# Kernel tuning notes

Hardware: AMD Instinct MI355X
Metric: run time of the kernel (lower is better)

## Reference

```python
import jax, jax.numpy as jnp
import numpy as np

TYPE_PANEL, TYPE_DIALOG, TYPE_CHAR = 1, 2, 3
NUM_ELEMS = 64  # max element index per type (panel count cap per page)
B, S, D = 8, 4096, 768
NPC, NDS = 4, 4  # num_panel_classes, num_dialog_shapes


def setup_inputs() -> dict:
    key = jax.random.key(0)
    ks = jax.random.split(key, 16)
    w = lambda k, shp: jax.random.normal(k, shp, dtype=jnp.float32) * 0.02
    return {
        "element_types": jax.random.randint(ks[0], (B, S), 0, 4, dtype=jnp.int32),
        "element_indices": jax.random.randint(ks[1], (B, S), 0, NUM_ELEMS, dtype=jnp.int32),
        "parent_panel_indices": jax.random.randint(ks[2], (B, S), 0, NUM_ELEMS, dtype=jnp.int32),
        "style_vector": jax.random.normal(ks[3], (B, 4), dtype=jnp.float32),
        "type_emb": w(ks[4], (4, D)),
        "index_emb": w(ks[5], (NUM_ELEMS, D)),
        "parent_emb": w(ks[6], (NUM_ELEMS, D)),
        "style_w": w(ks[7], (4, D)),
        "style_b": jnp.zeros((D,), jnp.float32),
        "ln_g": jnp.ones((D,), jnp.float32),
        "ln_b": jnp.zeros((D,), jnp.float32),
        "panel_w": w(ks[8], (D, NPC + 4)),
        "panel_b": jnp.zeros((NPC + 4,), jnp.float32),
        "dialog_w": w(ks[9], (2 * D, NDS + 4)),
        "dialog_b": jnp.zeros((NDS + 4,), jnp.float32),
        "char_w": w(ks[10], (2 * D, 4)),
        "char_b": jnp.zeros((4,), jnp.float32),
    }


def reference(element_types, element_indices, parent_panel_indices, style_vector,
              type_emb, index_emb, parent_emb, style_w, style_b, ln_g, ln_b,
              panel_w, panel_b, dialog_w, dialog_b, char_w, char_b):
    Bv, Sv = element_types.shape
    # --- TokenLayoutEncoder: embedding sum + style projection + LayerNorm ---
    x = type_emb[element_types] + index_emb[element_indices] + parent_emb[parent_panel_indices]
    x = x + (style_vector @ style_w + style_b)[:, None, :]
    mu = x.mean(-1, keepdims=True)
    var = ((x - mu) ** 2).mean(-1, keepdims=True)
    feats = (x - mu) * jax.lax.rsqrt(var + 1e-5) * ln_g + ln_b  # (B,S,D)

    # --- vectorized _build_parent_remap: orig panel idx -> kept panel order pos ---
    panel_mask = element_types == TYPE_PANEL                      # (B,S)
    kept = (jnp.cumsum(panel_mask, axis=1) - 1).astype(jnp.int32) # order pos of each panel token
    brow = jnp.arange(Bv, dtype=jnp.int32)[:, None]
    col = jnp.where(panel_mask, element_indices, NUM_ELEMS)       # dummy slot for non-panels
    remap = (jnp.full((Bv, NUM_ELEMS + 1), -1, jnp.int32)
             .at[brow, col].max(kept))[:, :NUM_ELEMS]             # (B, NUM_ELEMS)
    # kept panel order pos -> sequence position (for parent feature gather)
    slot = jnp.where(panel_mask, kept, Sv)
    seq_ids = jnp.broadcast_to(jnp.arange(Sv, dtype=jnp.int32), (Bv, Sv))
    pos_table = (jnp.zeros((Bv, Sv + 1), jnp.int32)
                 .at[brow, slot].set(seq_ids))[:, :Sv]            # (B,S)

    # --- parent_pos per token (DIALOG/CHAR only), -1 otherwise ---
    child_mask = (element_types == TYPE_DIALOG) | (element_types == TYPE_CHAR)
    ppos = jnp.where(child_mask,
                     jnp.take_along_axis(remap, parent_panel_indices, axis=1), -1)
    valid = ppos >= 0
    pseq = jnp.take_along_axis(pos_table, jnp.clip(ppos, 0, Sv - 1), axis=1)
    parent_feats = jnp.take_along_axis(feats, pseq[..., None], axis=1)
    parent_feats = parent_feats * valid[..., None].astype(feats.dtype)
    cat = jnp.concatenate([feats, parent_feats], axis=-1)         # (B,S,2D)

    # --- ParallelPredictionHeads, masked per token type ---
    panel_out = (feats @ panel_w + panel_b) * panel_mask[..., None].astype(feats.dtype)
    dmask = ((element_types == TYPE_DIALOG) & valid)[..., None].astype(feats.dtype)
    cmask = ((element_types == TYPE_CHAR) & valid)[..., None].astype(feats.dtype)
    dialog_out = (cat @ dialog_w + dialog_b) * dmask
    char_out = (cat @ char_w + char_b) * cmask
    return panel_out, dialog_out, char_out
```

## Files before the change

### kernel.cpp

```cpp
#include <hip/hip_runtime.h>

#define NB 8
#define NS 4096
#define ND 768

typedef float4 f4;

static __device__ __forceinline__ float wred(float v) {
    v += __shfl_xor(v, 32, 64);
    v += __shfl_xor(v, 16, 64);
    v += __shfl_xor(v, 8, 64);
    v += __shfl_xor(v, 4, 64);
    v += __shfl_xor(v, 2, 64);
    v += __shfl_xor(v, 1, 64);
    return v;
}

static __device__ __forceinline__ f4 ld4(const float* __restrict__ p, int i) {
    return ((const f4*)p)[i];
}

__global__ __launch_bounds__(256) void lp_pre(
    const int* __restrict__ et, const int* __restrict__ ei,
    const float* __restrict__ sv, const float* __restrict__ sw,
    const float* __restrict__ sb,
    int* __restrict__ table, float* __restrict__ sprj)
{
    if (blockIdx.x < 128) {
        int t = blockIdx.x * 256 + threadIdx.x;
        if (et[t] == 1) {
            int b = t >> 12;
            atomicMax(&table[b * 64 + ei[t]], t & (NS - 1));
        }
    } else {
        const int lane = threadIdx.x & 63;
        const int b = (blockIdx.x - 128) * 4 + (threadIdx.x >> 6);
        const float sv0 = sv[b*4+0], sv1 = sv[b*4+1], sv2 = sv[b*4+2], sv3 = sv[b*4+3];
        #pragma unroll
        for (int g = 0; g < 3; ++g) {
            int i = g*64 + lane;
            f4 w0 = ld4(sw, i), w1 = ld4(sw, 192+i), w2 = ld4(sw, 384+i), w3 = ld4(sw, 576+i);
            f4 bb = ld4(sb, i);
            f4 r;
            r.x = bb.x + sv0*w0.x + sv1*w1.x + sv2*w2.x + sv3*w3.x;
            r.y = bb.y + sv0*w0.y + sv1*w1.y + sv2*w2.y + sv3*w3.y;
            r.z = bb.z + sv0*w0.z + sv1*w1.z + sv2*w2.z + sv3*w3.z;
            r.w = bb.w + sv0*w0.w + sv1*w1.w + sv2*w2.w + sv3*w3.w;
            ((f4*)(sprj + b*ND))[i] = r;
        }
    }
}

__global__ __launch_bounds__(256) void lp_parent(
    const int* __restrict__ ei, const int* __restrict__ ppi,
    const float* __restrict__ temb, const float* __restrict__ iemb,
    const float* __restrict__ pemb, const float* __restrict__ lng,
    const float* __restrict__ lnb,
    const int* __restrict__ table, const float* __restrict__ sprj,
    float* __restrict__ pfeat)
{
    const int lane = threadIdx.x & 63;
    const int slot = blockIdx.x * 4 + (threadIdx.x >> 6);
    const int b = slot >> 6;
    const int pp = table[slot];
    if (pp < 0) return;
    const int ptok = b * NS + pp;
    const int pei = ei[ptok], pppi = ppi[ptok];
    const float* ie = iemb + pei * ND;
    const float* pe = pemb + pppi * ND;
    const float* sp = sprj + b * ND;

    f4 x[3]; float s1 = 0.f;
    #pragma unroll
    for (int g = 0; g < 3; ++g) {
        int i = g*64 + lane;
        f4 a = ld4(temb + ND, i), c = ld4(ie, i), d = ld4(pe, i), s = ld4(sp, i);
        x[g].x = a.x + c.x + d.x + s.x;
        x[g].y = a.y + c.y + d.y + s.y;
        x[g].z = a.z + c.z + d.z + s.z;
        x[g].w = a.w + c.w + d.w + s.w;
        s1 += x[g].x + x[g].y + x[g].z + x[g].w;
    }
    float mu = wred(s1) * (1.f/ND);
    float s2 = 0.f;
    #pragma unroll
    for (int g = 0; g < 3; ++g) {
        float dx = x[g].x-mu, dy = x[g].y-mu, dz = x[g].z-mu, dw_ = x[g].w-mu;
        s2 += dx*dx + dy*dy + dz*dz + dw_*dw_;
    }
    float rs = rsqrtf(wred(s2) * (1.f/ND) + 1e-5f);
    float* dst = pfeat + (size_t)slot * ND;
    #pragma unroll
    for (int g = 0; g < 3; ++g) {
        int i = g*64 + lane;
        f4 gg = ld4(lng, i), bb = ld4(lnb, i);
        f4 r;
        r.x = (x[g].x-mu)*rs*gg.x + bb.x;
        r.y = (x[g].y-mu)*rs*gg.y + bb.y;
        r.z = (x[g].z-mu)*rs*gg.z + bb.z;
        r.w = (x[g].w-mu)*rs*gg.w + bb.w;
        ((f4*)dst)[i] = r;
    }
}

__global__ __launch_bounds__(256) void lp_main(
    const int* __restrict__ et, const int* __restrict__ ei, const int* __restrict__ ppi,
    const float* __restrict__ temb, const float* __restrict__ iemb,
    const float* __restrict__ pemb, const float* __restrict__ lng,
    const float* __restrict__ lnb,
    const float* __restrict__ pw, const float* __restrict__ pb,
    const float* __restrict__ dw, const float* __restrict__ db,
    const float* __restrict__ cw, const float* __restrict__ cb,
    const int* __restrict__ table, const float* __restrict__ sprj,
    const float* __restrict__ pfeat,
    float* __restrict__ out)
{
    __shared__ float lds[4][2*ND];
    const int lane = threadIdx.x & 63;
    const int widx = threadIdx.x >> 6;
    const int t = blockIdx.x * 4 + widx;
    const int b = t >> 12;
    const int type = et[t];

    float pval = 0.f, dval = 0.f, cval = 0.f;

    if (type != 0) {
        const int my_ei = ei[t], my_ppi = ppi[t];
        float* fl = lds[widx];
        const float* te = temb + type * ND;
        const float* ie = iemb + my_ei * ND;
        const float* pe = pemb + my_ppi * ND;
        const float* sp = sprj + b * ND;

        f4 x[3]; float s1 = 0.f;
        #pragma unroll
        for (int g = 0; g < 3; ++g) {
            int i = g*64 + lane;
            f4 a = ld4(te, i), c = ld4(ie, i), d = ld4(pe, i), s = ld4(sp, i);
            x[g].x = a.x + c.x + d.x + s.x;
            x[g].y = a.y + c.y + d.y + s.y;
            x[g].z = a.z + c.z + d.z + s.z;
            x[g].w = a.w + c.w + d.w + s.w;
            s1 += x[g].x + x[g].y + x[g].z + x[g].w;
        }
        float mu = wred(s1) * (1.f/ND);
        float s2 = 0.f;
        #pragma unroll
        for (int g = 0; g < 3; ++g) {
            float dx = x[g].x-mu, dy = x[g].y-mu, dz = x[g].z-mu, dw_ = x[g].w-mu;
            s2 += dx*dx + dy*dy + dz*dz + dw_*dw_;
        }
        float rs = rsqrtf(wred(s2) * (1.f/ND) + 1e-5f);
        #pragma unroll
        for (int g = 0; g < 3; ++g) {
            int i = g*64 + lane;
            f4 gg = ld4(lng, i), bb = ld4(lnb, i);
            f4 r;
            r.x = (x[g].x-mu)*rs*gg.x + bb.x;
            r.y = (x[g].y-mu)*rs*gg.y + bb.y;
            r.z = (x[g].z-mu)*rs*gg.z + bb.z;
            r.w = (x[g].w-mu)*rs*gg.w + bb.w;
            ((f4*)fl)[i] = r;
        }

        if (type == 1) {
            const int di = lane >> 3;
            float acc = 0.f;
            #pragma unroll 16
            for (int s = 0; s < 96; ++s)
                acc += pw[s*64 + lane] * fl[s*8 + di];
            acc += __shfl_xor(acc, 8, 64);
            acc += __shfl_xor(acc, 16, 64);
            acc += __shfl_xor(acc, 32, 64);
            pval = acc + pb[lane & 7];
        } else {
            const int pp = table[b*64 + my_ppi];
            if (pp >= 0) {
                const float* pfr = pfeat + (size_t)(b*64 + my_ppi) * ND;
                #pragma unroll
                for (int g = 0; g < 3; ++g)
                    ((f4*)(fl + ND))[g*64 + lane] = ld4(pfr, g*64 + lane);

                if (type == 2) {
                    const int di = lane >> 3;
                    float acc = 0.f;
                    #pragma unroll 16
                    for (int s = 0; s < 192; ++s)
                        acc += dw[s*64 + lane] * fl[s*8 + di];
                    acc += __shfl_xor(acc, 8, 64);
                    acc += __shfl_xor(acc, 16, 64);
                    acc += __shfl_xor(acc, 32, 64);
                    dval = acc + db[lane & 7];
                } else {
                    const int di = lane >> 2;
                    float acc = 0.f;
                    #pragma unroll 16
                    for (int s = 0; s < 96; ++s)
                        acc += cw[s*64 + lane] * fl[s*16 + di];
                    acc += __shfl_xor(acc, 4, 64);
                    acc += __shfl_xor(acc, 8, 64);
                    acc += __shfl_xor(acc, 16, 64);
                    acc += __shfl_xor(acc, 32, 64);
                    cval = acc + cb[lane & 3];
                }
            }
        }
    }

    if (lane < 8) out[(size_t)t*8 + lane] = pval;
    if (lane < 8) out[(size_t)NB*NS*8 + (size_t)t*8 + lane] = dval;
    if (lane < 4) out[(size_t)NB*NS*16 + (size_t)t*4 + lane] = cval;
}

extern "C" void kernel_launch(void* const* d_in, const int* in_sizes, int n_in,
                              void* d_out, int out_size, void* d_ws, size_t ws_size,
                              hipStream_t stream) {
    const int* et  = (const int*)d_in[0];
    const int* ei  = (const int*)d_in[1];
    const int* ppi = (const int*)d_in[2];
    const float* sv   = (const float*)d_in[3];
    const float* temb = (const float*)d_in[4];
    const float* iemb = (const float*)d_in[5];
    const float* pemb = (const float*)d_in[6];
    const float* sw   = (const float*)d_in[7];
    const float* sb   = (const float*)d_in[8];
    const float* lng  = (const float*)d_in[9];
    const float* lnb  = (const float*)d_in[10];
    const float* pw   = (const float*)d_in[11];
    const float* pb   = (const float*)d_in[12];
    const float* dw   = (const float*)d_in[13];
    const float* db   = (const float*)d_in[14];
    const float* cw   = (const float*)d_in[15];
    const float* cbp  = (const float*)d_in[16];
    float* out = (float*)d_out;

    int*   table = (int*)d_ws;
    float* sprj  = (float*)((char*)d_ws + 4096);
    float* pfeat = (float*)((char*)d_ws + 32768);

    hipMemsetAsync(table, 0xFF, NB * 64 * sizeof(int), stream);

    lp_pre<<<130, 256, 0, stream>>>(et, ei, sv, sw, sb, table, sprj);
    lp_parent<<<128, 256, 0, stream>>>(ei, ppi, temb, iemb, pemb, lng, lnb,
                                       table, sprj, pfeat);
    lp_main<<<(NB*NS)/4, 256, 0, stream>>>(et, ei, ppi, temb, iemb, pemb,
                                           lng, lnb, pw, pb, dw, db, cw, cbp,
                                           table, sprj, pfeat, out);
}
```

Before: 139.4 us.

## Compact tokens per type and compute heads with bf16 MFMA tiles

Tokens are bucketed by type into lists using atomic counters, and per-type blocks process 16-token tiles. Each block stages the head weights into LDS as bf16 and runs the LayerNorm output and parent features through 16x16x32 bf16 MFMA instead of per-wave scalar dot products. Parent features are stored as bf16, the output is zeroed up front, and the LayerNorm uses single-pass variance. This aims to remove wasted work on type-0 tokens and the scalar matvec cost, but it lowers precision to bf16, adds atomics and repeats the weight staging in every block.

```diff
diff --git a/kernel.cpp b/kernel.cpp
--- a/kernel.cpp
+++ b/kernel.cpp
@@ -3,213 +3,257 @@
 #define NB 8
 #define NS 4096
 #define ND 768
+#define NT 32768
 
 typedef float4 f4;
-
-static __device__ __forceinline__ float wred(float v) {
-    v += __shfl_xor(v, 32, 64);
-    v += __shfl_xor(v, 16, 64);
-    v += __shfl_xor(v, 8, 64);
-    v += __shfl_xor(v, 4, 64);
-    v += __shfl_xor(v, 2, 64);
-    v += __shfl_xor(v, 1, 64);
-    return v;
-}
-
-static __device__ __forceinline__ f4 ld4(const float* __restrict__ p, int i) {
-    return ((const f4*)p)[i];
-}
-
-__global__ __launch_bounds__(256) void lp_pre(
+typedef __attribute__((ext_vector_type(8))) short short8;
+typedef __attribute__((ext_vector_type(4))) float floatx4;
+typedef unsigned short ushort_t;
+typedef unsigned int uint_t;
+
+static __device__ __forceinline__ ushort_t f2b(float f) {
+    union { float f; uint_t u; } v; v.f = f;
+    uint_t r = (v.u + 0x7FFFu + ((v.u >> 16) & 1u)) >> 16;
+    return (ushort_t)r;
+}
+static __device__ __forceinline__ float b2f(ushort_t s) {
+    union { uint_t u; float f; } v; v.u = ((uint_t)s) << 16;
+    return v.f;
+}
+static __device__ __forceinline__ f4 ld4(const float* p) { return *(const f4*)p; }
+
+__global__ __launch_bounds__(256) void k1(
     const int* __restrict__ et, const int* __restrict__ ei,
     const float* __restrict__ sv, const float* __restrict__ sw,
     const float* __restrict__ sb,
-    int* __restrict__ table, float* __restrict__ sprj)
+    int* __restrict__ table, float* __restrict__ sprj, float* __restrict__ out)
 {
+    const int tid = blockIdx.x * 256 + threadIdx.x;
+    for (int i = tid; i < 163840; i += 33280)
+        ((f4*)out)[i] = make_float4(0.f, 0.f, 0.f, 0.f);
+
     if (blockIdx.x < 128) {
-        int t = blockIdx.x * 256 + threadIdx.x;
-        if (et[t] == 1) {
-            int b = t >> 12;
-            atomicMax(&table[b * 64 + ei[t]], t & (NS - 1));
-        }
+        if (et[tid] == 1)
+            atomicMax(&table[(tid >> 12) * 64 + ei[tid]], tid & (NS - 1));
     } else {
         const int lane = threadIdx.x & 63;
         const int b = (blockIdx.x - 128) * 4 + (threadIdx.x >> 6);
-        const float sv0 = sv[b*4+0], sv1 = sv[b*4+1], sv2 = sv[b*4+2], sv3 = sv[b*4+3];
+        const float s0 = sv[b*4+0], s1 = sv[b*4+1], s2 = sv[b*4+2], s3 = sv[b*4+3];
         #pragma unroll
         for (int g = 0; g < 3; ++g) {
             int i = g*64 + lane;
-            f4 w0 = ld4(sw, i), w1 = ld4(sw, 192+i), w2 = ld4(sw, 384+i), w3 = ld4(sw, 576+i);
-            f4 bb = ld4(sb, i);
+            f4 w0 = ((const f4*)sw)[i],       w1 = ((const f4*)sw)[192+i];
+            f4 w2 = ((const f4*)sw)[384+i],   w3 = ((const f4*)sw)[576+i];
+            f4 bb = ((const f4*)sb)[i];
             f4 r;
-            r.x = bb.x + sv0*w0.x + sv1*w1.x + sv2*w2.x + sv3*w3.x;
-            r.y = bb.y + sv0*w0.y + sv1*w1.y + sv2*w2.y + sv3*w3.y;
-            r.z = bb.z + sv0*w0.z + sv1*w1.z + sv2*w2.z + sv3*w3.z;
-            r.w = bb.w + sv0*w0.w + sv1*w1.w + sv2*w2.w + sv3*w3.w;
+            r.x = bb.x + s0*w0.x + s1*w1.x + s2*w2.x + s3*w3.x;
+            r.y = bb.y + s0*w0.y + s1*w1.y + s2*w2.y + s3*w3.y;
+            r.z = bb.z + s0*w0.z + s1*w1.z + s2*w2.z + s3*w3.z;
+            r.w = bb.w + s0*w0.w + s1*w1.w + s2*w2.w + s3*w3.w;
             ((f4*)(sprj + b*ND))[i] = r;
         }
     }
 }
 
-__global__ __launch_bounds__(256) void lp_parent(
-    const int* __restrict__ ei, const int* __restrict__ ppi,
+__global__ __launch_bounds__(256) void k2(
+    const int* __restrict__ et, const int* __restrict__ ei, const int* __restrict__ ppi,
     const float* __restrict__ temb, const float* __restrict__ iemb,
     const float* __restrict__ pemb, const float* __restrict__ lng,
     const float* __restrict__ lnb,
     const int* __restrict__ table, const float* __restrict__ sprj,
-    float* __restrict__ pfeat)
+    ushort_t* __restrict__ pfeat, int* __restrict__ cnt, int* __restrict__ lists)
 {
-    const int lane = threadIdx.x & 63;
-    const int slot = blockIdx.x * 4 + (threadIdx.x >> 6);
-    const int b = slot >> 6;
-    const int pp = table[slot];
-    if (pp < 0) return;
-    const int ptok = b * NS + pp;
-    const int pei = ei[ptok], pppi = ppi[ptok];
-    const float* ie = iemb + pei * ND;
-    const float* pe = pemb + pppi * ND;
-    const float* sp = sprj + b * ND;
-
-    f4 x[3]; float s1 = 0.f;
-    #pragma unroll
-    for (int g = 0; g < 3; ++g) {
-        int i = g*64 + lane;
-        f4 a = ld4(temb + ND, i), c = ld4(ie, i), d = ld4(pe, i), s = ld4(sp, i);
-        x[g].x = a.x + c.x + d.x + s.x;
-        x[g].y = a.y + c.y + d.y + s.y;
-        x[g].z = a.z + c.z + d.z + s.z;
-        x[g].w = a.w + c.w + d.w + s.w;
-        s1 += x[g].x + x[g].y + x[g].z + x[g].w;
-    }
-    float mu = wred(s1) * (1.f/ND);
-    float s2 = 0.f;
-    #pragma unroll
-    for (int g = 0; g < 3; ++g) {
-        float dx = x[g].x-mu, dy = x[g].y-mu, dz = x[g].z-mu, dw_ = x[g].w-mu;
-        s2 += dx*dx + dy*dy + dz*dz + dw_*dw_;
-    }
-    float rs = rsqrtf(wred(s2) * (1.f/ND) + 1e-5f);
-    float* dst = pfeat + (size_t)slot * ND;
-    #pragma unroll
-    for (int g = 0; g < 3; ++g) {
-        int i = g*64 + lane;
-        f4 gg = ld4(lng, i), bb = ld4(lnb, i);
-        f4 r;
-        r.x = (x[g].x-mu)*rs*gg.x + bb.x;
-        r.y = (x[g].y-mu)*rs*gg.y + bb.y;
-        r.z = (x[g].z-mu)*rs*gg.z + bb.z;
-        r.w = (x[g].w-mu)*rs*gg.w + bb.w;
-        ((f4*)dst)[i] = r;
-    }
-}
-
-__global__ __launch_bounds__(256) void lp_main(
-    const int* __restrict__ et, const int* __restrict__ ei, const int* __restrict__ ppi,
+    if (blockIdx.x < 128) {
+        const int lane = threadIdx.x & 63;
+        const int slot = blockIdx.x * 4 + (threadIdx.x >> 6);
+        const int pp = table[slot];
+        if (pp < 0) return;
+        const int b = slot >> 6;
+        const int ptok = b * NS + pp;
+        const float* ie = iemb + ei[ptok] * ND;
+        const float* pe = pemb + ppi[ptok] * ND;
+        const float* sp = sprj + b * ND;
+
+        f4 x[3]; float s1 = 0.f;
+        #pragma unroll
+        for (int g = 0; g < 3; ++g) {
+            int i = g*64 + lane;
+            f4 a = ((const f4*)(temb + ND))[i], c = ((const f4*)ie)[i];
+            f4 d = ((const f4*)pe)[i],          s = ((const f4*)sp)[i];
+            x[g].x = a.x + c.x + d.x + s.x;
+            x[g].y = a.y + c.y + d.y + s.y;
+            x[g].z = a.z + c.z + d.z + s.z;
+            x[g].w = a.w + c.w + d.w + s.w;
+            s1 += x[g].x + x[g].y + x[g].z + x[g].w;
+        }
+        #pragma unroll
+        for (int o = 1; o < 64; o <<= 1) s1 += __shfl_xor(s1, o, 64);
+        float mu = s1 * (1.f/ND);
+        float s2 = 0.f;
+        #pragma unroll
+        for (int g = 0; g < 3; ++g) {
+            float dx = x[g].x-mu, dy = x[g].y-mu, dz = x[g].z-mu, dw_ = x[g].w-mu;
+            s2 += dx*dx + dy*dy + dz*dz + dw_*dw_;
+        }
+        #pragma unroll
+        for (int o = 1; o < 64; o <<= 1) s2 += __shfl_xor(s2, o, 64);
+        float rs = rsqrtf(s2 * (1.f/ND) + 1e-5f);
+        ushort_t* dst = pfeat + (size_t)slot * ND;
+        #pragma unroll
+        for (int g = 0; g < 3; ++g) {
+            int i = g*64 + lane;
+            f4 gg = ((const f4*)lng)[i], bb = ((const f4*)lnb)[i];
+            ushort_t r0 = f2b((x[g].x-mu)*rs*gg.x + bb.x);
+            ushort_t r1 = f2b((x[g].y-mu)*rs*gg.y + bb.y);
+            ushort_t r2 = f2b((x[g].z-mu)*rs*gg.z + bb.z);
+            ushort_t r3 = f2b((x[g].w-mu)*rs*gg.w + bb.w);
+            *(uint2*)(dst + 4*i) = make_uint2((uint_t)r0 | ((uint_t)r1 << 16),
+                                              (uint_t)r2 | ((uint_t)r3 << 16));
+        }
+    } else {
+        const int t = (blockIdx.x - 128) * 256 + threadIdx.x;
+        const int ty = et[t];
+        if (ty == 1) {
+            int idx = atomicAdd(&cnt[0], 1);
+            lists[idx] = t;
+        } else if (ty >= 2) {
+            if (table[(t >> 12) * 64 + ppi[t]] >= 0) {
+                int idx = atomicAdd(&cnt[ty-1], 1);
+                lists[(ty-1) * NT + idx] = t;
+            }
+        }
+    }
+}
+
+__global__ __launch_bounds__(256) void k3(
+    const int* __restrict__ ei, const int* __restrict__ ppi,
     const float* __restrict__ temb, const float* __restrict__ iemb,
     const float* __restrict__ pemb, const float* __restrict__ lng,
     const float* __restrict__ lnb,
     const float* __restrict__ pw, const float* __restrict__ pb,
     const float* __restrict__ dw, const float* __restrict__ db,
     const float* __restrict__ cw, const float* __restrict__ cb,
-    const int* __restrict__ table, const float* __restrict__ sprj,
-    const float* __restrict__ pfeat,
+    const float* __restrict__ sprj, const ushort_t* __restrict__ pfeat,
+    const int* __restrict__ cnt, const int* __restrict__ lists,
     float* __restrict__ out)
 {
-    __shared__ float lds[4][2*ND];
+    __shared__ uint4 bbuf[48 * 64];
+    const int ty = (blockIdx.x >> 9) + 1;
+    const int chunk = blockIdx.x & 511;
+    const int cn = cnt[ty - 1];
+    if (chunk * 64 >= cn) return;
+
+    const int W = (ty == 3) ? 4 : 8;
+    const int wsh = (ty == 3) ? 2 : 3;
+    const int Ktot = (ty == 1) ? 768 : 1536;
+    const float* wsrc = (ty == 1) ? pw : (ty == 2) ? dw : cw;
+    const float* bias = (ty == 1) ? pb : (ty == 2) ? db : cb;
+    const int* list = lists + (ty - 1) * NT;
+
+    const int nq = (Ktot / 32) * 64;
+    for (int i = threadIdx.x; i < nq; i += 256)
+        bbuf[i] = make_uint4(0u, 0u, 0u, 0u);
+    __syncthreads();
+    {
+        const int f4n = (Ktot * W) / 4;
+        for (int i = threadIdx.x; i < f4n; i += 256) {
+            f4 v = ((const f4*)wsrc)[i];
+            #pragma unroll
+            for (int q = 0; q < 4; ++q) {
+                int e = 4*i + q;
+                int k = e >> wsh, n = e & (W - 1);
+                int l = (((k >> 3) & 3) << 4) + n;
+                int s = k >> 5, j = k & 7;
+                float val = (q == 0) ? v.x : (q == 1) ? v.y : (q == 2) ? v.z : v.w;
+                ((ushort_t*)bbuf)[(s*64 + l)*8 + j] = f2b(val);
+            }
+        }
+    }
+    __syncthreads();
+
     const int lane = threadIdx.x & 63;
-    const int widx = threadIdx.x >> 6;
-    const int t = blockIdx.x * 4 + widx;
-    const int b = t >> 12;
-    const int type = et[t];
-
-    float pval = 0.f, dval = 0.f, cval = 0.f;
-
-    if (type != 0) {
-        const int my_ei = ei[t], my_ppi = ppi[t];
-        float* fl = lds[widx];
-        const float* te = temb + type * ND;
-        const float* ie = iemb + my_ei * ND;
-        const float* pe = pemb + my_ppi * ND;
-        const float* sp = sprj + b * ND;
-
-        f4 x[3]; float s1 = 0.f;
-        #pragma unroll
-        for (int g = 0; g < 3; ++g) {
-            int i = g*64 + lane;
-            f4 a = ld4(te, i), c = ld4(ie, i), d = ld4(pe, i), s = ld4(sp, i);
-            x[g].x = a.x + c.x + d.x + s.x;
-            x[g].y = a.y + c.y + d.y + s.y;
-            x[g].z = a.z + c.z + d.z + s.z;
-            x[g].w = a.w + c.w + d.w + s.w;
-            s1 += x[g].x + x[g].y + x[g].z + x[g].w;
-        }
-        float mu = wred(s1) * (1.f/ND);
-        float s2 = 0.f;
-        #pragma unroll
-        for (int g = 0; g < 3; ++g) {
-            float dx = x[g].x-mu, dy = x[g].y-mu, dz = x[g].z-mu, dw_ = x[g].w-mu;
-            s2 += dx*dx + dy*dy + dz*dz + dw_*dw_;
-        }
-        float rs = rsqrtf(wred(s2) * (1.f/ND) + 1e-5f);
-        #pragma unroll
-        for (int g = 0; g < 3; ++g) {
-            int i = g*64 + lane;
-            f4 gg = ld4(lng, i), bb = ld4(lnb, i);
-            f4 r;
-            r.x = (x[g].x-mu)*rs*gg.x + bb.x;
-            r.y = (x[g].y-mu)*rs*gg.y + bb.y;
-            r.z = (x[g].z-mu)*rs*gg.z + bb.z;
-            r.w = (x[g].w-mu)*rs*gg.w + bb.w;
-            ((f4*)fl)[i] = r;
-        }
-
-        if (type == 1) {
-            const int di = lane >> 3;
-            float acc = 0.f;
-            #pragma unroll 16
-            for (int s = 0; s < 96; ++s)
-                acc += pw[s*64 + lane] * fl[s*8 + di];
-            acc += __shfl_xor(acc, 8, 64);
-            acc += __shfl_xor(acc, 16, 64);
-            acc += __shfl_xor(acc, 32, 64);
-            pval = acc + pb[lane & 7];
-        } else {
-            const int pp = table[b*64 + my_ppi];
-            if (pp >= 0) {
-                const float* pfr = pfeat + (size_t)(b*64 + my_ppi) * ND;
-                #pragma unroll
-                for (int g = 0; g < 3; ++g)
-                    ((f4*)(fl + ND))[g*64 + lane] = ld4(pfr, g*64 + lane);
-
-                if (type == 2) {
-                    const int di = lane >> 3;
-                    float acc = 0.f;
-                    #pragma unroll 16
-                    for (int s = 0; s < 192; ++s)
-                        acc += dw[s*64 + lane] * fl[s*8 + di];
-                    acc += __shfl_xor(acc, 8, 64);
-                    acc += __shfl_xor(acc, 16, 64);
-                    acc += __shfl_xor(acc, 32, 64);
-                    dval = acc + db[lane & 7];
-                } else {
-                    const int di = lane >> 2;
-                    float acc = 0.f;
-                    #pragma unroll 16
-                    for (int s = 0; s < 96; ++s)
-                        acc += cw[s*64 + lane] * fl[s*16 + di];
-                    acc += __shfl_xor(acc, 4, 64);
-                    acc += __shfl_xor(acc, 8, 64);
-                    acc += __shfl_xor(acc, 16, 64);
-                    acc += __shfl_xor(acc, 32, 64);
-                    cval = acc + cb[lane & 3];
-                }
-            }
-        }
-    }
-
-    if (lane < 8) out[(size_t)t*8 + lane] = pval;
-    if (lane < 8) out[(size_t)NB*NS*8 + (size_t)t*8 + lane] = dval;
-    if (lane < 4) out[(size_t)NB*NS*16 + (size_t)t*4 + lane] = cval;
+    const int gbase = chunk * 64 + (threadIdx.x >> 6) * 16;
+    if (gbase >= cn) return;
+    const int m = lane & 15;
+    const int koff = (lane >> 4) * 8;
+    const int slot = min(gbase + m, cn - 1);
+    const int tl = list[slot];
+    const int b = tl >> 12;
+    const int eidx = ei[tl], pidx = ppi[tl];
+    const float* ie_p = iemb + eidx * ND;
+    const float* pe_p = pemb + pidx * ND;
+    const float* sp_p = sprj + b * ND;
+    const float* te_p = temb + ty * ND;
+
+    short8 xf[24];
+    float sum = 0.f, sq = 0.f;
+    #pragma unroll
+    for (int s = 0; s < 24; ++s) {
+        int d0 = 32*s + koff;
+        f4 a0 = ld4(te_p + d0), a1 = ld4(te_p + d0 + 4);
+        f4 c0 = ld4(ie_p + d0), c1 = ld4(ie_p + d0 + 4);
+        f4 e0 = ld4(pe_p + d0), e1 = ld4(pe_p + d0 + 4);
+        f4 p0 = ld4(sp_p + d0), p1 = ld4(sp_p + d0 + 4);
+        float x0 = a0.x + c0.x + e0.x + p0.x;
+        float x1 = a0.y + c0.y + e0.y + p0.y;
+        float x2 = a0.z + c0.z + e0.z + p0.z;
+        float x3 = a0.w + c0.w + e0.w + p0.w;
+        float x4 = a1.x + c1.x + e1.x + p1.x;
+        float x5 = a1.y + c1.y + e1.y + p1.y;
+        float x6 = a1.z + c1.z + e1.z + p1.z;
+        float x7 = a1.w + c1.w + e1.w + p1.w;
+        sum += (x0+x1)+(x2+x3)+(x4+x5)+(x6+x7);
+        sq  += (x0*x0+x1*x1)+(x2*x2+x3*x3)+(x4*x4+x5*x5)+(x6*x6+x7*x7);
+        short8 t8;
+        t8[0]=(short)f2b(x0); t8[1]=(short)f2b(x1); t8[2]=(short)f2b(x2); t8[3]=(short)f2b(x3);
+        t8[4]=(short)f2b(x4); t8[5]=(short)f2b(x5); t8[6]=(short)f2b(x6); t8[7]=(short)f2b(x7);
+        xf[s] = t8;
+    }
+    sum += __shfl_xor(sum, 16, 64); sum += __shfl_xor(sum, 32, 64);
+    sq  += __shfl_xor(sq , 16, 64); sq  += __shfl_xor(sq , 32, 64);
+    float mu = sum * (1.f/ND);
+    float rs = rsqrtf(sq * (1.f/ND) - mu*mu + 1e-5f);
+
+    floatx4 acc = {0.f, 0.f, 0.f, 0.f};
+    #pragma unroll
+    for (int s = 0; s < 24; ++s) {
+        int d0 = 32*s + koff;
+        f4 g0 = ld4(lng + d0), g1 = ld4(lng + d0 + 4);
+        f4 h0 = ld4(lnb + d0), h1 = ld4(lnb + d0 + 4);
+        short8 ff;
+        ff[0] = (short)f2b((b2f((ushort_t)xf[s][0]) - mu)*rs*g0.x + h0.x);
+        ff[1] = (short)f2b((b2f((ushort_t)xf[s][1]) - mu)*rs*g0.y + h0.y);
+        ff[2] = (short)f2b((b2f((ushort_t)xf[s][2]) - mu)*rs*g0.z + h0.z);
+        ff[3] = (short)f2b((b2f((ushort_t)xf[s][3]) - mu)*rs*g0.w + h0.w);
+        ff[4] = (short)f2b((b2f((ushort_t)xf[s][4]) - mu)*rs*g1.x + h1.x);
+        ff[5] = (short)f2b((b2f((ushort_t)xf[s][5]) - mu)*rs*g1.y + h1.y);
+        ff[6] = (short)f2b((b2f((ushort_t)xf[s][6]) - mu)*rs*g1.z + h1.z);
+        ff[7] = (short)f2b((b2f((ushort_t)xf[s][7]) - mu)*rs*g1.w + h1.w);
+        short8 bf = ((short8*)bbuf)[s*64 + lane];
+        acc = __builtin_amdgcn_mfma_f32_16x16x32_bf16(ff, bf, acc, 0, 0, 0);
+    }
+    if (ty != 1) {
+        const ushort_t* pf_p = pfeat + (size_t)(b*64 + pidx) * ND;
+        #pragma unroll
+        for (int s = 0; s < 24; ++s) {
+            short8 af = *(const short8*)(pf_p + 32*s + koff);
+            short8 bf = ((short8*)bbuf)[(24 + s)*64 + lane];
+            acc = __builtin_amdgcn_mfma_f32_16x16x32_bf16(af, bf, acc, 0, 0, 0);
+        }
+    }
+
+    const int n = lane & 15;
+    const float bv = (n < W) ? bias[n] : 0.f;
+    const long obase = (ty == 1) ? 0L : (ty == 2) ? (long)NT*8 : (long)NT*16;
+    #pragma unroll
+    for (int r = 0; r < 4; ++r) {
+        int row = (lane >> 4) * 4 + r;
+        int rslot = gbase + row;
+        if (n < W && rslot < cn) {
+            int tr = list[rslot];
+            out[obase + (long)tr * W + n] = acc[r] + bv;
+        }
+    }
 }
 
 extern "C" void kernel_launch(void* const* d_in, const int* in_sizes, int n_in,
@@ -234,16 +278,19 @@
     const float* cbp  = (const float*)d_in[16];
     float* out = (float*)d_out;
 
-    int*   table = (int*)d_ws;
-    float* sprj  = (float*)((char*)d_ws + 4096);
-    float* pfeat = (float*)((char*)d_ws + 32768);
-
-    hipMemsetAsync(table, 0xFF, NB * 64 * sizeof(int), stream);
-
-    lp_pre<<<130, 256, 0, stream>>>(et, ei, sv, sw, sb, table, sprj);
-    lp_parent<<<128, 256, 0, stream>>>(ei, ppi, temb, iemb, pemb, lng, lnb,
-                                       table, sprj, pfeat);
-    lp_main<<<(NB*NS)/4, 256, 0, stream>>>(et, ei, ppi, temb, iemb, pemb,
-                                           lng, lnb, pw, pb, dw, db, cw, cbp,
-                                           table, sprj, pfeat, out);
-}
+    int*      table = (int*)d_ws;
+    int*      cnt   = (int*)((char*)d_ws + 2048);
+    float*    sprj  = (float*)((char*)d_ws + 4096);
+    ushort_t* pfeat = (ushort_t*)((char*)d_ws + 28672);
+    int*      lists = (int*)((char*)d_ws + 815104);
+
+    hipMemsetAsync(table, 0xFF, 512 * sizeof(int), stream);
+    hipMemsetAsync(cnt, 0x00, 3 * sizeof(int), stream);
+
+    k1<<<130, 256, 0, stream>>>(et, ei, sv, sw, sb, table, sprj, out);
+    k2<<<256, 256, 0, stream>>>(et, ei, ppi, temb, iemb, pemb, lng, lnb,
+                                table, sprj, pfeat, cnt, lists);
+    k3<<<1536, 256, 0, stream>>>(ei, ppi, temb, iemb, pemb, lng, lnb,
+                                 pw, pb, dw, db, cw, cbp, sprj, pfeat,
+                                 cnt, lists, out);
+}
```

Measured after the change: 276.7 us. 1.99x slower.
